# Optimization experiments

Hardware: AMD Instinct MI355X
Metric: run time of the kernel (lower is better)

## Reference

```python
import jax, jax.numpy as jnp
import numpy as np

B, S, HID, NH = 2, 2048, 1024, 16
HD = HID // NH

def setup_inputs() -> dict:
    key = jax.random.key(0)
    ks = jax.random.split(key, 9)
    s = 1.0 / np.sqrt(HID)
    return {
        "hidden_state": jax.random.normal(ks[0], (B, S, HID), jnp.float32),
        "Wq": jax.random.normal(ks[1], (HID, HID), jnp.float32) * s,
        "bq": jax.random.normal(ks[2], (HID,), jnp.float32) * 0.02,
        "Wk": jax.random.normal(ks[3], (HID, HID), jnp.float32) * s,
        "bk": jax.random.normal(ks[4], (HID,), jnp.float32) * 0.02,
        "Wv": jax.random.normal(ks[5], (HID, HID), jnp.float32) * s,
        "bv": jax.random.normal(ks[6], (HID,), jnp.float32) * 0.02,
        "Wo": jax.random.normal(ks[7], (HID, HID), jnp.float32) * s,
        "bo": jax.random.normal(ks[8], (HID,), jnp.float32) * 0.02,
    }

def _split_heads(x):
    # [B,S,HID] -> [B,NH,S,HD]
    b, s, _ = x.shape
    return x.reshape(b, s, NH, HD).transpose(0, 2, 1, 3)

def reference(hidden_state, Wq, bq, Wk, bk, Wv, bv, Wo, bo):
    # torch nn.Linear: y = x @ W.T + b
    q = _split_heads(hidden_state @ Wq.T + bq)
    k = _split_heads(hidden_state @ Wk.T + bk)
    v = _split_heads(hidden_state @ Wv.T + bv)
    scale = 1.0 / jnp.sqrt(jnp.asarray(HD, hidden_state.dtype))
    scores = jnp.einsum("bhqd,bhkd->bhqk", q, k) * scale
    probs = jax.nn.softmax(scores, axis=-1)
    out = jnp.einsum("bhqk,bhkd->bhqd", probs, v)  # [B,NH,S,HD]
    out = out.transpose(0, 2, 1, 3).reshape(hidden_state.shape[0], -1, NH * HD)
    return out @ Wo.T + bo
```

## Files before the change

### kernel.cpp

```cpp
#include <hip/hip_runtime.h>


#define S_LEN 2048
#define HID   1024
#define NHEAD 16
#define HDIM  64
#define M_TOT 4096
#define LOG2E 1.4426950408889634f

typedef __attribute__((ext_vector_type(8))) short bf16x8;
typedef __attribute__((ext_vector_type(4))) float f32x4;

static __device__ __forceinline__ float b2f(short s) {
  union { unsigned int u; float f; } v;
  v.u = ((unsigned int)(unsigned short)s) << 16;
  return v.f;
}
static __device__ __forceinline__ short f2b(float f) {
  union { unsigned int u; float f; } v; v.f = f;
  unsigned int r = (v.u + 0x7FFFu + ((v.u >> 16) & 1u)) >> 16;
  return (short)(unsigned short)r;
}
static __device__ __forceinline__ short f2b_fast(float f) {
  union { unsigned int u; float f; } v; v.f = f;
  return (short)(unsigned short)((v.u + 0x8000u) >> 16);
}
static __device__ __forceinline__ float fexp2(float x) { return exp2f(x); }

#define GLD_LDS16(g, l)                                                        \
  __builtin_amdgcn_global_load_lds(                                            \
      (const __attribute__((address_space(1))) void*)(g),                      \
      (__attribute__((address_space(3))) void*)(l), 16, 0, 0)

__global__ __launch_bounds__(256) void convert_all_kernel(
    const float* s0, const float* s1, const float* s2, const float* s3,
    const float* s4, const float* s5, const float* s6, const float* s7,
    const float* s8,
    short* d0, short* d1, short* d2, short* d3, short* d4,
    short* d5, short* d6, short* d7, short* d8)
{
  const float* src; short* dst; int n;
  switch (blockIdx.y) {
    case 0: src = s0; dst = d0; n = M_TOT * HID; break;
    case 1: src = s1; dst = d1; n = HID * HID; break;
    case 2: src = s2; dst = d2; n = HID; break;
    case 3: src = s3; dst = d3; n = HID * HID; break;
    case 4: src = s4; dst = d4; n = HID; break;
    case 5: src = s5; dst = d5; n = HID * HID; break;
    case 6: src = s6; dst = d6; n = HID; break;
    case 7: src = s7; dst = d7; n = HID * HID; break;
    default: src = s8; dst = d8; n = HID; break;
  }
  const int stride = gridDim.x * 256 * 4;
  int i = (blockIdx.x * 256 + threadIdx.x) * 4;
  for (; i < n; i += stride) {
    float4 v = *(const float4*)(src + i);
    ushort4 o;
    o.x = (unsigned short)f2b(v.x); o.y = (unsigned short)f2b(v.y);
    o.z = (unsigned short)f2b(v.z); o.w = (unsigned short)f2b(v.w);
    *(ushort4*)(dst + i) = o;
  }
}

__global__ __launch_bounds__(256) void gemm_qkv_kernel(
    const short* __restrict__ X,
    const short* __restrict__ Wq, const short* __restrict__ Wk, const short* __restrict__ Wv,
    const short* __restrict__ bq, const short* __restrict__ bk, const short* __restrict__ bv,
    short* __restrict__ Q, short* __restrict__ K, short* __restrict__ V)
{
  __shared__ short Alds[8704];
  __shared__ short Wlds[64 * 64];
  const int ntile = blockIdx.y;
  const int which = ntile >> 4;
  const int n0    = (ntile & 15) * 64;
  const int bm    = blockIdx.x * 128;
  const short* W    = (which == 0) ? Wq : (which == 1) ? Wk : Wv;
  const short* bias = (which == 0) ? bq : (which == 1) ? bk : bv;

  const int t    = threadIdx.x;
  const int lane = t & 63;
  const int w    = t >> 6;
  const int quad = lane >> 4, l15 = lane & 15;

  f32x4 acc[2][4];
#pragma unroll
  for (int i = 0; i < 2; ++i)
#pragma unroll
    for (int j = 0; j < 4; ++j) acc[i][j] = (f32x4){0.f, 0.f, 0.f, 0.f};

  {
    const int srow = t >> 3;
    const int cg   = (t & 7) ^ (srow & 7);
    const short* Ag = X + (size_t)(bm + srow) * HID + cg * 8;
    const short* Wg = W + (size_t)(n0 + srow) * HID + cg * 8;

    for (int k0 = 0; k0 < HID; k0 += 64) {
      __syncthreads();
#pragma unroll
      for (int i = 0; i < 4; ++i)
        GLD_LDS16(Ag + (size_t)i * 32 * HID + k0, Alds + i * 2048 + t * 8);
#pragma unroll
      for (int i = 0; i < 2; ++i)
        GLD_LDS16(Wg + (size_t)i * 32 * HID + k0, Wlds + i * 2048 + t * 8);
      __syncthreads();

      bf16x8 af[2][2], bfr[4][2];
#pragma unroll
      for (int mt = 0; mt < 2; ++mt)
#pragma unroll
        for (int ks = 0; ks < 2; ++ks)
          af[mt][ks] = *(const bf16x8*)(Alds + (w * 32 + mt * 16 + l15) * 64 +
                                        (((ks * 4 + quad) ^ (l15 & 7)) * 8));
#pragma unroll
      for (int nt = 0; nt < 4; ++nt)
#pragma unroll
        for (int ks = 0; ks < 2; ++ks)
          bfr[nt][ks] = *(const bf16x8*)(Wlds + (nt * 16 + l15) * 64 +
                                         (((ks * 4 + quad) ^ (l15 & 7)) * 8));
#pragma unroll
      for (int mt = 0; mt < 2; ++mt)
#pragma unroll
        for (int nt = 0; nt < 4; ++nt) {
          acc[mt][nt] = __builtin_amdgcn_mfma_f32_16x16x32_bf16(af[mt][0], bfr[nt][0], acc[mt][nt], 0, 0, 0);
          acc[mt][nt] = __builtin_amdgcn_mfma_f32_16x16x32_bf16(af[mt][1], bfr[nt][1], acc[mt][nt], 0, 0, 0);
        }
    }
  }

  if (which != 2) {
    short* Out = (which == 0) ? Q : K;
    const float scl = (which == 0) ? 0.125f * LOG2E : 1.0f;
#pragma unroll
    for (int nt = 0; nt < 4; ++nt) {
      const int n = n0 + nt * 16 + l15;
      const float bvv = b2f(bias[n]);
#pragma unroll
      for (int mt = 0; mt < 2; ++mt)
#pragma unroll
        for (int r = 0; r < 4; ++r) {
          const int m = bm + w * 32 + mt * 16 + quad * 4 + r;
          Out[(size_t)m * HID + n] = f2b((acc[mt][nt][r] + bvv) * scl);
        }
    }
  } else {
    __syncthreads();
#pragma unroll
    for (int nt = 0; nt < 4; ++nt) {
      const int n = nt * 16 + l15;
      const float bvv = b2f(bias[n0 + n]);
#pragma unroll
      for (int mt = 0; mt < 2; ++mt) {
        const int m = w * 32 + mt * 16 + quad * 4;
#pragma unroll
        for (int r = 0; r < 4; r += 2) {
          union { unsigned int u; short s2[2]; } pk;
          pk.s2[0] = f2b(acc[mt][nt][r] + bvv);
          pk.s2[1] = f2b(acc[mt][nt][r + 1] + bvv);
          *(unsigned int*)(Alds + n * 136 + m + r) = pk.u;
        }
      }
    }
    __syncthreads();
    const int nr   = t >> 2;
    const int mseg = (t & 3) * 32;
    const int bb = bm >> 11, s0 = bm & 2047;
    short* dst = V + ((size_t)(bb * 1024 + n0 + nr)) * 2048 + s0 + mseg;
#pragma unroll
    for (int k = 0; k < 4; ++k)
      *(bf16x8*)(dst + k * 8) = *(const bf16x8*)(Alds + nr * 136 + mseg + k * 8);
  }
}

__global__ __launch_bounds__(256) void gemm_o_kernel(
    const short* __restrict__ A, const short* __restrict__ W,
    const short* __restrict__ bias, float* __restrict__ out)
{
  __shared__ short Alds[128 * 64];
  __shared__ short Wlds[64 * 64];
  const int n0 = blockIdx.y * 64;
  const int bm = blockIdx.x * 128;

  const int t    = threadIdx.x;
  const int lane = t & 63;
  const int w    = t >> 6;
  const int quad = lane >> 4, l15 = lane & 15;

  f32x4 acc[2][4];
#pragma unroll
  for (int i = 0; i < 2; ++i)
#pragma unroll
    for (int j = 0; j < 4; ++j) acc[i][j] = (f32x4){0.f, 0.f, 0.f, 0.f};

  const int srow = t >> 3;
  const int cg   = (t & 7) ^ (srow & 7);
  const short* Ag = A + (size_t)(bm + srow) * HID + cg * 8;
  const short* Wg = W + (size_t)(n0 + srow) * HID + cg * 8;

  for (int k0 = 0; k0 < HID; k0 += 64) {
    __syncthreads();
#pragma unroll
    for (int i = 0; i < 4; ++i)
      GLD_LDS16(Ag + (size_t)i * 32 * HID + k0, Alds + i * 2048 + t * 8);
#pragma unroll
    for (int i = 0; i < 2; ++i)
      GLD_LDS16(Wg + (size_t)i * 32 * HID + k0, Wlds + i * 2048 + t * 8);
    __syncthreads();

    bf16x8 af[2][2], bfr[4][2];
#pragma unroll
    for (int mt = 0; mt < 2; ++mt)
#pragma unroll
      for (int ks = 0; ks < 2; ++ks)
        af[mt][ks] = *(const bf16x8*)(Alds + (w * 32 + mt * 16 + l15) * 64 +
                                      (((ks * 4 + quad) ^ (l15 & 7)) * 8));
#pragma unroll
    for (int nt = 0; nt < 4; ++nt)
#pragma unroll
      for (int ks = 0; ks < 2; ++ks)
        bfr[nt][ks] = *(const bf16x8*)(Wlds + (nt * 16 + l15) * 64 +
                                       (((ks * 4 + quad) ^ (l15 & 7)) * 8));
#pragma unroll
    for (int mt = 0; mt < 2; ++mt)
#pragma unroll
      for (int nt = 0; nt < 4; ++nt) {
        acc[mt][nt] = __builtin_amdgcn_mfma_f32_16x16x32_bf16(af[mt][0], bfr[nt][0], acc[mt][nt], 0, 0, 0);
        acc[mt][nt] = __builtin_amdgcn_mfma_f32_16x16x32_bf16(af[mt][1], bfr[nt][1], acc[mt][nt], 0, 0, 0);
      }
  }

#pragma unroll
  for (int nt = 0; nt < 4; ++nt) {
    const int n = n0 + nt * 16 + l15;
    const float bvv = b2f(bias[n]);
#pragma unroll
    for (int mt = 0; mt < 2; ++mt)
#pragma unroll
      for (int r = 0; r < 4; ++r) {
        const int m = bm + w * 32 + mt * 16 + quad * 4 + r;
        out[(size_t)m * HID + n] = acc[mt][nt][r] + bvv;
      }
  }
}

__global__ __launch_bounds__(256) void flash_attn_kernel(
    const short* __restrict__ Q, const short* __restrict__ K,
    const short* __restrict__ V, short* __restrict__ O)
{
  __shared__ short Kl0[64 * 64], Kl1[64 * 64];
  __shared__ short Vl0[64 * 64], Vl1[64 * 64];
  __shared__ short Pl[4 * 32 * 64];

  const int t    = threadIdx.x;
  const int lane = t & 63, w = t >> 6;
  const int quad = lane >> 4, l15 = lane & 15;
  const int qtile = blockIdx.x;
  const int bh    = blockIdx.y;
  const int b = bh >> 4, h = bh & 15;
  const int hoff = h * HDIM;

  bf16x8 qf[2][2];
#pragma unroll
  for (int mt = 0; mt < 2; ++mt) {
    const int qrow = b * S_LEN + qtile * 128 + w * 32 + mt * 16 + l15;
#pragma unroll
    for (int ks = 0; ks < 2; ++ks)
      qf[mt][ks] = *(const bf16x8*)(Q + (size_t)qrow * HID + hoff + ks * 32 + quad * 8);
  }

  f32x4 o[2][4], ol[2];
#pragma unroll
  for (int mt = 0; mt < 2; ++mt) {
#pragma unroll
    for (int nt = 0; nt < 4; ++nt) o[mt][nt] = (f32x4){0.f, 0.f, 0.f, 0.f};
    ol[mt] = (f32x4){0.f, 0.f, 0.f, 0.f};
  }

  bf16x8 vones;
#pragma unroll
  for (int j = 0; j < 8; ++j) vones[j] = (short)0x3F80;

  short* myP = Pl + w * (32 * 64);
  const int srow = t >> 3;
  const int cg   = (t & 7) ^ (srow & 7);
  const short* Kg = K + (size_t)(b * S_LEN) * HID + hoff + cg * 8;
  const short* Vg = V + (size_t)(bh * HDIM) * S_LEN + cg * 8;

  auto stage = [&](short* dK, short* dV, int kv0) {
    GLD_LDS16(Kg + (size_t)(kv0 + srow) * HID,      dK + t * 8);
    GLD_LDS16(Kg + (size_t)(kv0 + 32 + srow) * HID, dK + 2048 + t * 8);
    GLD_LDS16(Vg + (size_t)srow * S_LEN + kv0,        dV + t * 8);
    GLD_LDS16(Vg + (size_t)(32 + srow) * S_LEN + kv0, dV + 2048 + t * 8);
  };

  auto step = [&](int it, const short* Kc, const short* Vc, short* Kn, short* Vn) {
    __syncthreads();
    if (it < 31) stage(Kn, Vn, (it + 1) * 64);

    bf16x8 kf[4][2];
#pragma unroll
    for (int kt = 0; kt < 4; ++kt)
#pragma unroll
      for (int ks = 0; ks < 2; ++ks)
        kf[kt][ks] = *(const bf16x8*)(Kc + (kt * 16 + l15) * 64 +
                                      (((ks * 4 + quad) ^ (l15 & 7)) * 8));

#pragma unroll
    for (int mt = 0; mt < 2; ++mt) {
      f32x4 s[4];
#pragma unroll
      for (int kt = 0; kt < 4; ++kt) {
        s[kt] = (f32x4){0.f, 0.f, 0.f, 0.f};
        s[kt] = __builtin_amdgcn_mfma_f32_16x16x32_bf16(qf[mt][0], kf[kt][0], s[kt], 0, 0, 0);
        s[kt] = __builtin_amdgcn_mfma_f32_16x16x32_bf16(qf[mt][1], kf[kt][1], s[kt], 0, 0, 0);
      }
      short* Pm = myP + mt * (16 * 64);
#pragma unroll
      for (int kt = 0; kt < 4; ++kt)
#pragma unroll
        for (int r = 0; r < 4; ++r)
          Pm[(quad * 4 + r) * 64 + (((kt * 2 + (l15 >> 3)) ^ quad) * 8) + (l15 & 7)] =
              f2b_fast(fexp2(s[kt][r]));
    }

    bf16x8 pa[2][2];
#pragma unroll
    for (int mt = 0; mt < 2; ++mt)
#pragma unroll
      for (int ks = 0; ks < 2; ++ks)
        pa[mt][ks] = *(const bf16x8*)(myP + (mt * 16 + l15) * 64 +
                                      (((ks * 4 + quad) ^ ((l15 >> 2) & 3)) * 8));

#pragma unroll
    for (int nt = 0; nt < 4; ++nt) {
#pragma unroll
      for (int ks = 0; ks < 2; ++ks) {
        bf16x8 vf = *(const bf16x8*)(Vc + (nt * 16 + l15) * 64 +
                                     (((ks * 4 + quad) ^ (l15 & 7)) * 8));
        o[0][nt] = __builtin_amdgcn_mfma_f32_16x16x32_bf16(pa[0][ks], vf, o[0][nt], 0, 0, 0);
        o[1][nt] = __builtin_amdgcn_mfma_f32_16x16x32_bf16(pa[1][ks], vf, o[1][nt], 0, 0, 0);
      }
    }
#pragma unroll
    for (int mt = 0; mt < 2; ++mt) {
      ol[mt] = __builtin_amdgcn_mfma_f32_16x16x32_bf16(pa[mt][0], vones, ol[mt], 0, 0, 0);
      ol[mt] = __builtin_amdgcn_mfma_f32_16x16x32_bf16(pa[mt][1], vones, ol[mt], 0, 0, 0);
    }
  };

  stage(Kl0, Vl0, 0);
#pragma unroll 1
  for (int it = 0; it < 32; it += 2) {
    step(it,     Kl0, Vl0, Kl1, Vl1);
    step(it + 1, Kl1, Vl1, Kl0, Vl0);
  }

#pragma unroll
  for (int mt = 0; mt < 2; ++mt) {
    const int orow = b * S_LEN + qtile * 128 + w * 32 + mt * 16 + quad * 4;
#pragma unroll
    for (int nt = 0; nt < 4; ++nt) {
      const int col = hoff + nt * 16 + l15;
#pragma unroll
      for (int r = 0; r < 4; ++r)
        O[(size_t)(orow + r) * HID + col] = f2b(o[mt][nt][r] / ol[mt][r]);
    }
  }
}

extern "C" void kernel_launch(void* const* d_in, const int* in_sizes, int n_in,
                              void* d_out, int out_size, void* d_ws, size_t ws_size,
                              hipStream_t stream) {
  short* WS  = (short*)d_ws;
  const size_t M1 = 1024 * 1024;
  short* Xc  = WS;
  short* Wqc = WS + 4 * M1;
  short* Wkc = WS + 5 * M1;
  short* Wvc = WS + 6 * M1;
  short* Woc = WS + 7 * M1;
  short* bqc = WS + 8 * M1;
  short* bkc = bqc + 1024;
  short* bvc = bkc + 1024;
  short* boc = bvc + 1024;
  short* Qb  = WS + 9 * M1;
  short* Kb  = WS + 13 * M1;
  short* Vt  = WS + 17 * M1;
  short* An  = WS + 21 * M1;

  convert_all_kernel<<<dim3(128, 9), 256, 0, stream>>>(
      (const float*)d_in[0], (const float*)d_in[1], (const float*)d_in[2],
      (const float*)d_in[3], (const float*)d_in[4], (const float*)d_in[5],
      (const float*)d_in[6], (const float*)d_in[7], (const float*)d_in[8],
      Xc, Wqc, bqc, Wkc, bkc, Wvc, bvc, Woc, boc);

  gemm_qkv_kernel<<<dim3(32, 48), 256, 0, stream>>>(
      Xc, Wqc, Wkc, Wvc, bqc, bkc, bvc, Qb, Kb, Vt);

  flash_attn_kernel<<<dim3(16, 32), 256, 0, stream>>>(Qb, Kb, Vt, An);

  gemm_o_kernel<<<dim3(32, 16), 256, 0, stream>>>(An, Woc, boc, (float*)d_out);
}
```

Baseline: 209.9 us.

## Halve attention query tile to 64 rows and remap blocks so heads share K/V

The flash attention kernel now gives each block 64 query rows instead of 128, with each wave handling 16 rows, and launches twice as many blocks (1024). Block indices are remapped so that 8 consecutive blocks cover different heads at the same query tile. This raises parallelism and occupancy on the many-CU GPU and cuts per-wave registers and P scratch. In exchange, each K/V tile staged into LDS feeds half as many queries, so total K/V global traffic doubles.

Result: slower. 223.9 us (+6.7%).

```diff
diff --git a/kernel.cpp b/kernel.cpp
--- a/kernel.cpp
+++ b/kernel.cpp
@@ -248,38 +248,38 @@
 {
   __shared__ short Kl0[64 * 64], Kl1[64 * 64];
   __shared__ short Vl0[64 * 64], Vl1[64 * 64];
-  __shared__ short Pl[4 * 32 * 64];
+  __shared__ short Pl[4 * 16 * 64];
 
   const int t    = threadIdx.x;
   const int lane = t & 63, w = t >> 6;
   const int quad = lane >> 4, l15 = lane & 15;
-  const int qtile = blockIdx.x;
-  const int bh    = blockIdx.y;
+
+  const int lid   = blockIdx.x + (blockIdx.y << 5);
+  const int x8    = lid & 7;
+  const int rest  = lid >> 3;
+  const int bh    = x8 + ((rest >> 5) << 3);
+  const int qtile = rest & 31;
   const int b = bh >> 4, h = bh & 15;
   const int hoff = h * HDIM;
 
-  bf16x8 qf[2][2];
-#pragma unroll
-  for (int mt = 0; mt < 2; ++mt) {
-    const int qrow = b * S_LEN + qtile * 128 + w * 32 + mt * 16 + l15;
+  bf16x8 qf[2];
+  {
+    const int qrow = b * S_LEN + qtile * 64 + w * 16 + l15;
 #pragma unroll
     for (int ks = 0; ks < 2; ++ks)
-      qf[mt][ks] = *(const bf16x8*)(Q + (size_t)qrow * HID + hoff + ks * 32 + quad * 8);
-  }
-
-  f32x4 o[2][4], ol[2];
-#pragma unroll
-  for (int mt = 0; mt < 2; ++mt) {
-#pragma unroll
-    for (int nt = 0; nt < 4; ++nt) o[mt][nt] = (f32x4){0.f, 0.f, 0.f, 0.f};
-    ol[mt] = (f32x4){0.f, 0.f, 0.f, 0.f};
-  }
+      qf[ks] = *(const bf16x8*)(Q + (size_t)qrow * HID + hoff + ks * 32 + quad * 8);
+  }
+
+  f32x4 o[4], ol;
+#pragma unroll
+  for (int nt = 0; nt < 4; ++nt) o[nt] = (f32x4){0.f, 0.f, 0.f, 0.f};
+  ol = (f32x4){0.f, 0.f, 0.f, 0.f};
 
   bf16x8 vones;
 #pragma unroll
   for (int j = 0; j < 8; ++j) vones[j] = (short)0x3F80;
 
-  short* myP = Pl + w * (32 * 64);
+  short* myP = Pl + w * (16 * 64);
   const int srow = t >> 3;
   const int cg   = (t & 7) ^ (srow & 7);
   const short* Kg = K + (size_t)(b * S_LEN) * HID + hoff + cg * 8;
@@ -304,31 +304,25 @@
         kf[kt][ks] = *(const bf16x8*)(Kc + (kt * 16 + l15) * 64 +
                                       (((ks * 4 + quad) ^ (l15 & 7)) * 8));
 
-#pragma unroll
-    for (int mt = 0; mt < 2; ++mt) {
-      f32x4 s[4];
-#pragma unroll
-      for (int kt = 0; kt < 4; ++kt) {
-        s[kt] = (f32x4){0.f, 0.f, 0.f, 0.f};
-        s[kt] = __builtin_amdgcn_mfma_f32_16x16x32_bf16(qf[mt][0], kf[kt][0], s[kt], 0, 0, 0);
-        s[kt] = __builtin_amdgcn_mfma_f32_16x16x32_bf16(qf[mt][1], kf[kt][1], s[kt], 0, 0, 0);
-      }
-      short* Pm = myP + mt * (16 * 64);
-#pragma unroll
-      for (int kt = 0; kt < 4; ++kt)
-#pragma unroll
-        for (int r = 0; r < 4; ++r)
-          Pm[(quad * 4 + r) * 64 + (((kt * 2 + (l15 >> 3)) ^ quad) * 8) + (l15 & 7)] =
-              f2b_fast(fexp2(s[kt][r]));
-    }
-
-    bf16x8 pa[2][2];
-#pragma unroll
-    for (int mt = 0; mt < 2; ++mt)
-#pragma unroll
-      for (int ks = 0; ks < 2; ++ks)
-        pa[mt][ks] = *(const bf16x8*)(myP + (mt * 16 + l15) * 64 +
-                                      (((ks * 4 + quad) ^ ((l15 >> 2) & 3)) * 8));
+    f32x4 s[4];
+#pragma unroll
+    for (int kt = 0; kt < 4; ++kt) {
+      s[kt] = (f32x4){0.f, 0.f, 0.f, 0.f};
+      s[kt] = __builtin_amdgcn_mfma_f32_16x16x32_bf16(qf[0], kf[kt][0], s[kt], 0, 0, 0);
+      s[kt] = __builtin_amdgcn_mfma_f32_16x16x32_bf16(qf[1], kf[kt][1], s[kt], 0, 0, 0);
+    }
+#pragma unroll
+    for (int kt = 0; kt < 4; ++kt)
+#pragma unroll
+      for (int r = 0; r < 4; ++r)
+        myP[(quad * 4 + r) * 64 + (((kt * 2 + (l15 >> 3)) ^ quad) * 8) + (l15 & 7)] =
+            f2b_fast(fexp2(s[kt][r]));
+
+    bf16x8 pa[2];
+#pragma unroll
+    for (int ks = 0; ks < 2; ++ks)
+      pa[ks] = *(const bf16x8*)(myP + l15 * 64 +
+                                (((ks * 4 + quad) ^ ((l15 >> 2) & 3)) * 8));
 
 #pragma unroll
     for (int nt = 0; nt < 4; ++nt) {
@@ -336,15 +330,11 @@
       for (int ks = 0; ks < 2; ++ks) {
         bf16x8 vf = *(const bf16x8*)(Vc + (nt * 16 + l15) * 64 +
                                      (((ks * 4 + quad) ^ (l15 & 7)) * 8));
-        o[0][nt] = __builtin_amdgcn_mfma_f32_16x16x32_bf16(pa[0][ks], vf, o[0][nt], 0, 0, 0);
-        o[1][nt] = __builtin_amdgcn_mfma_f32_16x16x32_bf16(pa[1][ks], vf, o[1][nt], 0, 0, 0);
+        o[nt] = __builtin_amdgcn_mfma_f32_16x16x32_bf16(pa[ks], vf, o[nt], 0, 0, 0);
       }
     }
-#pragma unroll
-    for (int mt = 0; mt < 2; ++mt) {
-      ol[mt] = __builtin_amdgcn_mfma_f32_16x16x32_bf16(pa[mt][0], vones, ol[mt], 0, 0, 0);
-      ol[mt] = __builtin_amdgcn_mfma_f32_16x16x32_bf16(pa[mt][1], vones, ol[mt], 0, 0, 0);
-    }
+    ol = __builtin_amdgcn_mfma_f32_16x16x32_bf16(pa[0], vones, ol, 0, 0, 0);
+    ol = __builtin_amdgcn_mfma_f32_16x16x32_bf16(pa[1], vones, ol, 0, 0, 0);
   };
 
   stage(Kl0, Vl0, 0);
@@ -354,16 +344,13 @@
     step(it + 1, Kl1, Vl1, Kl0, Vl0);
   }
 
-#pragma unroll
-  for (int mt = 0; mt < 2; ++mt) {
-    const int orow = b * S_LEN + qtile * 128 + w * 32 + mt * 16 + quad * 4;
-#pragma unroll
-    for (int nt = 0; nt < 4; ++nt) {
-      const int col = hoff + nt * 16 + l15;
-#pragma unroll
-      for (int r = 0; r < 4; ++r)
-        O[(size_t)(orow + r) * HID + col] = f2b(o[mt][nt][r] / ol[mt][r]);
-    }
+  const int orow = b * S_LEN + qtile * 64 + w * 16 + quad * 4;
+#pragma unroll
+  for (int nt = 0; nt < 4; ++nt) {
+    const int col = hoff + nt * 16 + l15;
+#pragma unroll
+    for (int r = 0; r < 4; ++r)
+      O[(size_t)(orow + r) * HID + col] = f2b(o[nt][r] / ol[r]);
   }
 }
 
@@ -395,7 +382,7 @@
   gemm_qkv_kernel<<<dim3(32, 48), 256, 0, stream>>>(
       Xc, Wqc, Wkc, Wvc, bqc, bkc, bvc, Qb, Kb, Vt);
 
-  flash_attn_kernel<<<dim3(16, 32), 256, 0, stream>>>(Qb, Kb, Vt, An);
+  flash_attn_kernel<<<dim3(32, 32), 256, 0, stream>>>(Qb, Kb, Vt, An);
 
   gemm_o_kernel<<<dim3(32, 16), 256, 0, stream>>>(An, Woc, boc, (float*)d_out);
 }
```
